# Optimization experiments

Measured on AMD Instinct MI355X. Metric: run time of the kernel, lower is better.

## Reference

```python
import jax, jax.numpy as jnp
import numpy as np

BS, NQ, D = 4, 12500, 256
HEADS, LEVELS, POINTS = 8, 2, 4
HD = D // HEADS
D_FF = 2048
SHAPES = ((100, 100), (50, 50))   # (H, W) per level; sum(H*W) == NQ
STARTS = (0, 10000)


def layer_norm(x, g, b, eps=1e-5):
    m = x.mean(-1, keepdims=True)
    v = ((x - m) ** 2).mean(-1, keepdims=True)
    return (x - m) * jax.lax.rsqrt(v + eps) * g + b


def bilinear_sample(value_l, loc, H, W):
    # value_l: (bs, heads, H*W, hd); loc: (bs, heads, nq, P, 2) normalized [0,1]
    # matches F.grid_sample(align_corners=False, padding_mode='zeros')
    x = loc[..., 0] * W - 0.5
    y = loc[..., 1] * H - 0.5
    x0 = jnp.floor(x)
    y0 = jnp.floor(y)
    wx1 = x - x0
    wy1 = y - y0
    wx0 = 1.0 - wx1
    wy0 = 1.0 - wy1
    x0i = x0.astype(jnp.int32)
    y0i = y0.astype(jnp.int32)

    def gather(xi, yi):
        valid = (xi >= 0) & (xi < W) & (yi >= 0) & (yi < H)
        idx = jnp.clip(yi, 0, H - 1) * W + jnp.clip(xi, 0, W - 1)  # (bs,heads,nq,P)
        b, h, nq, P = idx.shape
        g = jnp.take_along_axis(value_l, idx.reshape(b, h, nq * P, 1), axis=2)
        g = g.reshape(b, h, nq, P, -1)
        return g * valid[..., None].astype(g.dtype)

    g00 = gather(x0i, y0i)
    g10 = gather(x0i + 1, y0i)
    g01 = gather(x0i, y0i + 1)
    g11 = gather(x0i + 1, y0i + 1)
    return (g00 * (wx0 * wy0)[..., None] + g10 * (wx1 * wy0)[..., None]
            + g01 * (wx0 * wy1)[..., None] + g11 * (wx1 * wy1)[..., None])


def setup_inputs() -> dict:
    key = jax.random.key(0)
    ks = jax.random.split(key, 20)
    s = 0.02
    inp = {
        'query': jax.random.normal(ks[0], (BS, NQ, D), jnp.float32),
        'reference_points': jax.random.uniform(ks[1], (BS, NQ, LEVELS, 2), jnp.float32),
        'w_off': s * jax.random.normal(ks[2], (D, HEADS * LEVELS * POINTS * 2), jnp.float32),
        'b_off': s * jax.random.normal(ks[3], (HEADS * LEVELS * POINTS * 2,), jnp.float32),
        'w_attn': s * jax.random.normal(ks[4], (D, HEADS * LEVELS * POINTS), jnp.float32),
        'b_attn': s * jax.random.normal(ks[5], (HEADS * LEVELS * POINTS,), jnp.float32),
        'w_val': s * jax.random.normal(ks[6], (D, D), jnp.float32),
        'b_val': jnp.zeros((D,), jnp.float32),
        'w_out': s * jax.random.normal(ks[7], (D, D), jnp.float32),
        'b_out': jnp.zeros((D,), jnp.float32),
        'w1': s * jax.random.normal(ks[8], (D, D_FF), jnp.float32),
        'b1': jnp.zeros((D_FF,), jnp.float32),
        'w2': s * jax.random.normal(ks[9], (D_FF, D), jnp.float32),
        'b2': jnp.zeros((D,), jnp.float32),
        'ln0_g': jnp.ones((D,), jnp.float32),
        'ln0_b': jnp.zeros((D,), jnp.float32),
        'ln1_g': jnp.ones((D,), jnp.float32),
        'ln1_b': jnp.zeros((D,), jnp.float32),
    }
    return inp


def reference(query, reference_points, w_off, b_off, w_attn, b_attn, w_val, b_val,
              w_out, b_out, w1, b1, w2, b2, ln0_g, ln0_b, ln1_g, ln1_b):
    bs, nq, _ = query.shape
    # value projection; encoder self-attention: value == query tokens
    value = (query @ w_val + b_val).reshape(bs, nq, HEADS, HD).transpose(0, 2, 1, 3)  # (bs,heads,nv,hd)
    off = (query @ w_off + b_off).reshape(bs, nq, HEADS, LEVELS, POINTS, 2)
    aw = (query @ w_attn + b_attn).reshape(bs, nq, HEADS, LEVELS * POINTS)
    aw = jax.nn.softmax(aw, axis=-1).reshape(bs, nq, HEADS, LEVELS, POINTS)

    out = jnp.zeros((bs, HEADS, nq, HD), query.dtype)
    for l, (H, W) in enumerate(SHAPES):
        normalizer = jnp.array([W, H], query.dtype)
        # (bs,nq,heads,P,2)
        loc = reference_points[:, :, None, l, None, :] + off[:, :, :, l] / normalizer
        loc = loc.transpose(0, 2, 1, 3, 4)  # (bs,heads,nq,P,2)
        v_l = value[:, :, STARTS[l]:STARTS[l] + H * W]  # (bs,heads,H*W,hd)
        sampled = bilinear_sample(v_l, loc, H, W)       # (bs,heads,nq,P,hd)
        w_l = aw[:, :, :, l].transpose(0, 2, 1, 3)      # (bs,heads,nq,P)
        out = out + (sampled * w_l[..., None]).sum(axis=3)

    attn_out = out.transpose(0, 2, 1, 3).reshape(bs, nq, D) @ w_out + b_out
    x = layer_norm(query + attn_out, ln0_g, ln0_b)
    h = jax.nn.relu(x @ w1 + b1)
    x = layer_norm(x + (h @ w2 + b2), ln1_g, ln1_b)
    return x
```

## Files before the change

kernel.cpp:

```cpp
#include <hip/hip_runtime.h>


#define NQv 12500
#define BSv 4
#define Dv  256
#define DFF 2048

typedef __attribute__((ext_vector_type(8))) __bf16 bf16x8;
typedef __attribute__((ext_vector_type(4))) float f32x4;

__device__ __forceinline__ ushort f32_to_bf16(float f) {
  unsigned u = __float_as_uint(f);
  u += 0x7FFFu + ((u >> 16) & 1u);
  return (ushort)(u >> 16);
}
__device__ __forceinline__ float bf16_to_f32(ushort u) {
  return __uint_as_float(((unsigned)u) << 16);
}

__global__ __launch_bounds__(256) void conv_bf16_kernel(
    const float* __restrict__ in, ushort* __restrict__ out, int n4) {
  int i = blockIdx.x * 256 + threadIdx.x;
  if (i >= n4) return;
  float4 v = reinterpret_cast<const float4*>(in)[i];
  uint2 st;
  st.x = (unsigned)f32_to_bf16(v.x) | ((unsigned)f32_to_bf16(v.y) << 16);
  st.y = (unsigned)f32_to_bf16(v.z) | ((unsigned)f32_to_bf16(v.w) << 16);
  reinterpret_cast<uint2*>(out)[i] = st;
}

__global__ __launch_bounds__(256) void ttrans_kernel(
    const float* __restrict__ in, ushort* __restrict__ out, int K, int N) {
  __shared__ ushort tl[64][65];
  const int n0 = blockIdx.x * 64, k0 = blockIdx.y * 64;
  const int t = threadIdx.x;
#pragma unroll
  for (int i = 0; i < 16; ++i) {
    int idx = t + 256 * i;
    int r = idx >> 6, c = idx & 63;
    tl[r][c] = f32_to_bf16(in[(size_t)(k0 + r) * N + n0 + c]);
  }
  __syncthreads();
#pragma unroll
  for (int i = 0; i < 16; ++i) {
    int idx = t + 256 * i;
    int r = idx >> 6, c = idx & 63;
    out[(size_t)(n0 + r) * K + k0 + c] = tl[c][r];
  }
}

__global__ __launch_bounds__(256) void build_wcat_kernel(
    const float* __restrict__ w_val, const float* __restrict__ w_off,
    const float* __restrict__ w_attn, const float* __restrict__ b_val,
    const float* __restrict__ b_off, const float* __restrict__ b_attn,
    ushort* __restrict__ wcat, float* __restrict__ bcat) {
  int i = blockIdx.x * 256 + threadIdx.x;
  if (i < 448 * 256) {
    int n = i >> 8, k = i & 255;
    float v = (n < 256) ? w_val[(size_t)k * 256 + n]
              : (n < 384) ? w_off[(size_t)k * 128 + (n - 256)]
                          : w_attn[(size_t)k * 64 + (n - 384)];
    wcat[i] = f32_to_bf16(v);
  }
  if (i < 512)
    bcat[i] = (i < 256) ? b_val[i] : (i < 384) ? b_off[i - 256]
              : (i < 448) ? b_attn[i - 384] : 0.f;
}

template <int MODE>
__global__ __launch_bounds__(256) void stagefmt_kernel(
    const ushort* __restrict__ src, ushort* __restrict__ dst) {
  int i = blockIdx.x * 256 + threadIdx.x;
  int g = i >> 10, c = i & 1023;
  int srcrow, srck;
  if (MODE == 0) { srcrow = (g >> 2) * 128 + (c & 127); srck = (g & 3) * 64 + ((c >> 7) & 7) * 8; }
  if (MODE == 1) { srcrow = c & 255; srck = (g >> 2) * 128 + (g & 3) * 32 + ((c >> 8) & 3) * 8; }
  if (MODE == 2) { srcrow = c & 255; srck = g * 32 + ((c >> 8) & 3) * 8; }
  const int LD = (MODE == 1) ? 2048 : 256;
  *reinterpret_cast<uint4*>(dst + (size_t)i * 8) =
      *reinterpret_cast<const uint4*>(src + (size_t)srcrow * LD + srck);
}

#define TBM 128
#define TBN 128
#define TBK 32

template <int RELU, int NMASK, int SPLIT>
__global__ __launch_bounds__(256) void gemm128_kernel(
    const ushort* __restrict__ A, const ushort* __restrict__ Bt,
    const float* __restrict__ bias, ushort* __restrict__ C,
    ushort* __restrict__ C2,
    int M, int K, int ldc, int Nreal) {
  __shared__ ushort lds[4][TBM * TBK];

  const int t = threadIdx.x;
  const int wid = t >> 6, lane = t & 63;
  const int wr = wid >> 1, wc = wid & 1;
  const int m0 = blockIdx.y * TBM;
  const int n0 = blockIdx.x * TBN;

  int srowA[2], srowB[2], gsl[2];
#pragma unroll
  for (int i = 0; i < 2; i++) {
    int row = i * 64 + (t >> 2);
    int ar = m0 + row;
    srowA[i] = (ar < M) ? ar : (M - 1);
    srowB[i] = n0 + row;
    gsl[i] = ((t & 3) ^ ((row >> 1) & 3)) * 8;
  }

  f32x4 acc[4][4] = {};
  const int nt = K / TBK;
  int cur = 0;

#pragma unroll
  for (int i = 0; i < 2; i++) {
    const int ldsoff = (i * 256 + wid * 64) * 8;
    __builtin_amdgcn_global_load_lds(
        (const __attribute__((address_space(1))) void*)(A + (size_t)srowA[i] * K + gsl[i]),
        (__attribute__((address_space(3))) void*)(lds[0] + ldsoff), 16, 0, 0);
    __builtin_amdgcn_global_load_lds(
        (const __attribute__((address_space(1))) void*)(Bt + (size_t)srowB[i] * K + gsl[i]),
        (__attribute__((address_space(3))) void*)(lds[1] + ldsoff), 16, 0, 0);
  }
  __syncthreads();

  const int rl = lane & 15, kh = lane >> 4;
  for (int tk = 0; tk < nt; ++tk) {
    if (tk + 1 < nt) {
      const int k0 = (tk + 1) * TBK;
      const int nb = (cur ^ 1) * 2;
#pragma unroll
      for (int i = 0; i < 2; i++) {
        const int ldsoff = (i * 256 + wid * 64) * 8;
        __builtin_amdgcn_global_load_lds(
            (const __attribute__((address_space(1))) void*)(A + (size_t)srowA[i] * K + k0 + gsl[i]),
            (__attribute__((address_space(3))) void*)(lds[nb] + ldsoff), 16, 0, 0);
        __builtin_amdgcn_global_load_lds(
            (const __attribute__((address_space(1))) void*)(Bt + (size_t)srowB[i] * K + k0 + gsl[i]),
            (__attribute__((address_space(3))) void*)(lds[nb + 1] + ldsoff), 16, 0, 0);
      }
    }
    {
      const ushort* As = lds[cur * 2];
      const ushort* Bs = lds[cur * 2 + 1];
      bf16x8 afr[4], bfr[4];
#pragma unroll
      for (int ni = 0; ni < 4; ni++) {
        int rowb = wc * 64 + ni * 16 + rl;
        int p = kh ^ ((rowb >> 1) & 3);
        bfr[ni] = *reinterpret_cast<const bf16x8*>(Bs + rowb * 32 + p * 8);
      }
#pragma unroll
      for (int mi = 0; mi < 4; mi++) {
        int rowa = wr * 64 + mi * 16 + rl;
        int p = kh ^ ((rowa >> 1) & 3);
        afr[mi] = *reinterpret_cast<const bf16x8*>(As + rowa * 32 + p * 8);
      }
#pragma unroll
      for (int mi = 0; mi < 4; mi++)
#pragma unroll
        for (int ni = 0; ni < 4; ni++)
          acc[mi][ni] = __builtin_amdgcn_mfma_f32_16x16x32_bf16(afr[mi], bfr[ni], acc[mi][ni], 0, 0, 0);
    }
    __syncthreads();
    cur ^= 1;
  }

  ushort* ldsC = lds[0];
  const int rgrp = lane >> 4, cl = lane & 15;
#pragma unroll
  for (int pass = 0; pass < 2; ++pass) {
    if (wr == pass) {
#pragma unroll
      for (int mi = 0; mi < 4; mi++) {
#pragma unroll
        for (int ni = 0; ni < 4; ni++) {
          int col = wc * 64 + ni * 16 + cl;
          float bv = bias[n0 + col];
#pragma unroll
          for (int r = 0; r < 4; r++) {
            int rloc = mi * 16 + rgrp * 4 + r;
            float v = acc[mi][ni][r] + bv;
            if (RELU) v = fmaxf(v, 0.f);
            ldsC[rloc * 132 + col] = f32_to_bf16(v);
          }
        }
      }
    }
    __syncthreads();
    {
      int rloc = t >> 2;
      int row = m0 + pass * 64 + rloc;
      if (row < M) {
#pragma unroll
        for (int j = 0; j < 4; j++) {
          int col = (t & 3) * 32 + j * 8;
          uint4 v = *reinterpret_cast<const uint4*>(ldsC + rloc * 132 + col);
          if (SPLIT) {
            int gcol = n0 + col;
            if (gcol < 256)
              *reinterpret_cast<uint4*>(C + (size_t)row * 256 + gcol) = v;
            else if (gcol < 448)
              *reinterpret_cast<uint4*>(C2 + (size_t)row * 192 + (gcol - 256)) = v;
          } else if (!NMASK || n0 + col < Nreal) {
            *reinterpret_cast<uint4*>(C + (size_t)row * ldc + n0 + col) = v;
          }
        }
      }
    }
    __syncthreads();
  }
}

__global__ __launch_bounds__(256, 2) void outproj_ln0_kernel(
    const ushort* __restrict__ samp,
    const ushort* __restrict__ wqf,
    const float* __restrict__ bias,
    const float* __restrict__ query,
    const float* __restrict__ g0, const float* __restrict__ be0,
    ushort* __restrict__ xb,
    int M) {
  __shared__ ushort lds_all[32768];
  ushort* As = lds_all;
  ushort* ring0 = lds_all + 16384;

  const int t = threadIdx.x;
  const int wv = t >> 6;
  const int lane = t & 63;
  const int rl = lane & 15, kq = lane >> 4;
  const int cl = lane & 15, g4 = lane >> 4;
  const int m0 = blockIdx.x * 64;

  ushort* ring[2] = {ring0, ring0 + 8192};

  auto issueB = [&](int j, ushort* dst) {
#pragma unroll
    for (int ii = 0; ii < 4; ++ii) {
      int c = t + 256 * ii;
      __builtin_amdgcn_global_load_lds(
          (const __attribute__((address_space(1))) void*)(wqf + (size_t)j * 8192 + (size_t)c * 8),
          (__attribute__((address_space(3))) void*)(dst + (size_t)c * 8), 16, 0, 0);
    }
  };

#pragma unroll
  for (int ii = 0; ii < 8; ++ii) {
    int c = t + 256 * ii;
    __builtin_amdgcn_global_load_lds(
        (const __attribute__((address_space(1))) void*)(
            samp + (size_t)blockIdx.x * 16384 + (size_t)c * 8),
        (__attribute__((address_space(3))) void*)(As + (size_t)c * 8), 16, 0, 0);
  }
  issueB(0, ring[0]);
  __syncthreads();

  f32x4 accF[4][4] = {};
  int cur = 0;

#pragma unroll
  for (int j = 0; j < 8; ++j) {
    if (j + 1 < 8) issueB(j + 1, ring[cur ^ 1]);
    const ushort* Bs = ring[cur];
    bf16x8 afr[4], bfr[4];
#pragma unroll
    for (int mi = 0; mi < 4; mi++)
      afr[mi] = *reinterpret_cast<const bf16x8*>(As + (j * 4 + kq) * 512 + (mi * 16 + rl) * 8);
#pragma unroll
    for (int ni = 0; ni < 4; ni++)
      bfr[ni] = *reinterpret_cast<const bf16x8*>(Bs + kq * 2048 + (wv * 64 + ni * 16 + rl) * 8);
    __builtin_amdgcn_s_setprio(1);
#pragma unroll
    for (int mi = 0; mi < 4; mi++)
#pragma unroll
      for (int ni = 0; ni < 4; ni++)
        accF[mi][ni] = __builtin_amdgcn_mfma_f32_16x16x32_bf16(afr[mi], bfr[ni], accF[mi][ni], 0, 0, 0);
    __builtin_amdgcn_s_setprio(0);
    __syncthreads();
    cur ^= 1;
  }

  float* ptab = (float*)ring0;
  float* mtab = (float*)(ring0 + 2048);

  float bc[4], gc[4], bec[4];
#pragma unroll
  for (int ni = 0; ni < 4; ni++) {
    int col = wv * 64 + ni * 16 + cl;
    bc[ni] = bias[col]; gc[ni] = g0[col]; bec[ni] = be0[col];
  }
#pragma unroll
  for (int mi = 0; mi < 4; mi++) {
#pragma unroll
    for (int ni = 0; ni < 4; ni++) {
      int col = wv * 64 + ni * 16 + cl;
#pragma unroll
      for (int r = 0; r < 4; r++) {
        int row = mi * 16 + g4 * 4 + r;
        int qrow = m0 + row; qrow = (qrow < M) ? qrow : (M - 1);
        accF[mi][ni][r] += bc[ni] + query[(size_t)qrow * 256 + col];
      }
    }
  }
#pragma unroll
  for (int mi = 0; mi < 4; mi++) {
#pragma unroll
    for (int r = 0; r < 4; r++) {
      float s = accF[mi][0][r] + accF[mi][1][r] + accF[mi][2][r] + accF[mi][3][r];
      float sq = accF[mi][0][r] * accF[mi][0][r] + accF[mi][1][r] * accF[mi][1][r] +
                 accF[mi][2][r] * accF[mi][2][r] + accF[mi][3][r] * accF[mi][3][r];
#pragma unroll
      for (int o = 1; o < 16; o <<= 1) {
        s += __shfl_xor(s, o, 64);
        sq += __shfl_xor(sq, o, 64);
      }
      if (cl == 0) {
        int row = mi * 16 + g4 * 4 + r;
        ptab[(row * 4 + wv) * 2 + 0] = s;
        ptab[(row * 4 + wv) * 2 + 1] = sq;
      }
    }
  }
  __syncthreads();
  {
    int row = t >> 2, part = t & 3;
    float s = ptab[(row * 4 + part) * 2 + 0];
    float sq = ptab[(row * 4 + part) * 2 + 1];
    s += __shfl_xor(s, 1, 64);  sq += __shfl_xor(sq, 1, 64);
    s += __shfl_xor(s, 2, 64);  sq += __shfl_xor(sq, 2, 64);
    if (part == 0) {
      float mean = s * (1.f / 256.f);
      float var = sq * (1.f / 256.f) - mean * mean;
      mtab[row * 2 + 0] = mean;
      mtab[row * 2 + 1] = rsqrtf(var + 1e-5f);
    }
  }
  __syncthreads();
#pragma unroll
  for (int mi = 0; mi < 4; mi++) {
#pragma unroll
    for (int r = 0; r < 4; r++) {
      int row = mi * 16 + g4 * 4 + r;
      float2 ms = *reinterpret_cast<const float2*>(mtab + row * 2);
      int grow = m0 + row;
      if (grow < M) {
        size_t base = (size_t)(grow >> 7) * 32768 + (size_t)(grow & 127) * 8;
#pragma unroll
        for (int ni = 0; ni < 4; ni++) {
          int col = wv * 64 + ni * 16 + cl;
          xb[base + (size_t)(col >> 3) * 1024 + (col & 7)] =
              f32_to_bf16((accF[mi][ni][r] - ms.x) * ms.y * gc[ni] + bec[ni]);
        }
      }
    }
  }
}

__global__ __launch_bounds__(512, 1) void ffn_ln_fused_kernel(
    const ushort* __restrict__ xb,
    const ushort* __restrict__ w1f,
    const float* __restrict__ b1,
    const ushort* __restrict__ w2f,
    const float* __restrict__ b2,
    const float* __restrict__ g1, const float* __restrict__ be1,
    float* __restrict__ out, int M) {
  __shared__ ushort lds_all[73856];
  ushort* As = lds_all;
  ushort* Hs = lds_all + 32768;
  ushort* stg0 = lds_all + 49280;

  const int t = threadIdx.x;
  const int wv = t >> 6;
  const int wm = wv >> 2;
  const int wn = wv & 3;
  const int lane = t & 63;
  const int rl = lane & 15, kq = lane >> 4;
  const int cl = lane & 15, g4 = lane >> 4;
  const int m0 = blockIdx.x * 128;

  auto stg = [&](int i) { return stg0 + i * 8192; };

  auto issueB1 = [&](int p, int j, ushort* dst) {
    const ushort* src = w1f + (size_t)(p * 4 + j) * 8192;
#pragma unroll
    for (int ii = 0; ii < 2; ++ii) {
      int c = t + 512 * ii;
      __builtin_amdgcn_global_load_lds(
          (const __attribute__((address_space(1))) void*)(src + (size_t)c * 8),
          (__attribute__((address_space(3))) void*)(dst + (size_t)c * 8), 16, 0, 0);
    }
  };
  auto issueB2 = [&](int p, int tt, ushort* dst) {
    const ushort* src = w2f + (size_t)(p * 4 + tt) * 8192;
#pragma unroll
    for (int ii = 0; ii < 2; ++ii) {
      int c = t + 512 * ii;
      __builtin_amdgcn_global_load_lds(
          (const __attribute__((address_space(1))) void*)(src + (size_t)c * 8),
          (__attribute__((address_space(3))) void*)(dst + (size_t)c * 8), 16, 0, 0);
    }
  };

#pragma unroll
  for (int ii = 0; ii < 8; ++ii) {
    int c = t + 512 * ii;
    __builtin_amdgcn_global_load_lds(
        (const __attribute__((address_space(1))) void*)(
            xb + (size_t)blockIdx.x * 32768 + (size_t)c * 8),
        (__attribute__((address_space(3))) void*)(As + (size_t)c * 8), 16, 0, 0);
  }
  issueB1(0, 0, stg(0));
  issueB1(0, 1, stg(1));
  asm volatile("s_waitcnt vmcnt(2)" ::: "memory");
  __builtin_amdgcn_s_barrier();

  f32x4 acc1[4][2] = {};
  f32x4 accF[4][4] = {};
  int cur = 0;

  for (int p = 0; p < 16; ++p) {
#pragma unroll
    for (int j = 0; j < 8; ++j) {
      int tgt = cur + 2; if (tgt >= 3) tgt -= 3;
      if (j <= 5) {
        const int j2 = j + 2;
        const int p2 = p + (j2 >> 3);
        if ((j2 & 7) < 4) issueB1(p2, j2 & 3, stg(tgt));
        else issueB2(p2, (j2 & 7) - 4, stg(tgt));
        asm volatile("s_waitcnt vmcnt(4) lgkmcnt(0)" ::: "memory");
      } else if (p < 15) {
        const int j2m = (j + 2) & 7;
        issueB1(p + 1, j2m, stg(tgt));
        asm volatile("s_waitcnt vmcnt(4) lgkmcnt(0)" ::: "memory");
      } else if (j == 6) {
        asm volatile("s_waitcnt vmcnt(2) lgkmcnt(0)" ::: "memory");
      } else {
        asm volatile("s_waitcnt vmcnt(0) lgkmcnt(0)" ::: "memory");
      }
      __builtin_amdgcn_s_barrier();
      __builtin_amdgcn_sched_barrier(0);

      const ushort* Bs = stg(cur);
      if (j < 4) {
        __builtin_amdgcn_s_setprio(1);
#pragma unroll
        for (int kk = 0; kk < 2; ++kk) {
          bf16x8 afr[4], bfr[2];
          const int slotA = j * 8 + kk * 4 + kq;
#pragma unroll
          for (int mi = 0; mi < 4; mi++)
            afr[mi] = *reinterpret_cast<const bf16x8*>(
                As + slotA * 1024 + (wm * 64 + mi * 16 + rl) * 8);
          const int slotB = kk * 4 + kq;
#pragma unroll
          for (int ni = 0; ni < 2; ni++)
            bfr[ni] = *reinterpret_cast<const bf16x8*>(
                Bs + slotB * 1024 + (wn * 32 + ni * 16 + rl) * 8);
#pragma unroll
          for (int mi = 0; mi < 4; mi++)
#pragma unroll
            for (int ni = 0; ni < 2; ni++)
              acc1[mi][ni] = __builtin_amdgcn_mfma_f32_16x16x32_bf16(afr[mi], bfr[ni], acc1[mi][ni], 0, 0, 0);
        }
        __builtin_amdgcn_s_setprio(0);
        if (j == 3) {
#pragma unroll
          for (int ni = 0; ni < 2; ni++) {
            int col = wn * 32 + ni * 16 + cl;
            float b1v = b1[p * 128 + col];
            const int s = col >> 3, w8 = col & 7;
#pragma unroll
            for (int mi = 0; mi < 4; mi++) {
#pragma unroll
              for (int r = 0; r < 4; r++) {
                int row = wm * 64 + mi * 16 + g4 * 4 + r;
                Hs[s * 1032 + row * 8 + w8] = f32_to_bf16(fmaxf(acc1[mi][ni][r] + b1v, 0.f));
              }
            }
          }
#pragma unroll
          for (int mi = 0; mi < 4; mi++)
#pragma unroll
            for (int ni = 0; ni < 2; ni++)
              acc1[mi][ni] = (f32x4){0.f, 0.f, 0.f, 0.f};
        }
      } else {
        const int tt = j - 4;
        bf16x8 a2f[4], b2f[4];
#pragma unroll
        for (int mi = 0; mi < 4; mi++)
          a2f[mi] = *reinterpret_cast<const bf16x8*>(
              Hs + (tt * 4 + kq) * 1032 + (wm * 64 + mi * 16 + rl) * 8);
#pragma unroll
        for (int ni = 0; ni < 4; ni++)
          b2f[ni] = *reinterpret_cast<const bf16x8*>(
              Bs + kq * 2048 + (wn * 64 + ni * 16 + rl) * 8);
        __builtin_amdgcn_s_setprio(1);
#pragma unroll
        for (int mi = 0; mi < 4; mi++)
#pragma unroll
          for (int ni = 0; ni < 4; ni++)
            accF[mi][ni] = __builtin_amdgcn_mfma_f32_16x16x32_bf16(a2f[mi], b2f[ni], accF[mi][ni], 0, 0, 0);
        __builtin_amdgcn_s_setprio(0);
      }
      cur = cur + 1; if (cur >= 3) cur -= 3;
    }
  }

  float* ptab = (float*)stg0;
  float* mtab = (float*)(stg0 + 2048);

  float b2c[4], g1c[4], bec[4];
#pragma unroll
  for (int ni = 0; ni < 4; ni++) {
    int col = wn * 64 + ni * 16 + cl;
    b2c[ni] = b2[col]; g1c[ni] = g1[col]; bec[ni] = be1[col];
  }
#pragma unroll
  for (int mi = 0; mi < 4; mi++) {
#pragma unroll
    for (int ni = 0; ni < 4; ni++) {
      int col = wn * 64 + ni * 16 + cl;
#pragma unroll
      for (int r = 0; r < 4; r++) {
        int row = wm * 64 + mi * 16 + g4 * 4 + r;
        ushort xv = As[(col >> 3) * 1024 + row * 8 + (col & 7)];
        accF[mi][ni][r] += b2c[ni] + bf16_to_f32(xv);
      }
    }
  }
#pragma unroll
  for (int mi = 0; mi < 4; mi++) {
#pragma unroll
    for (int r = 0; r < 4; r++) {
      float s = accF[mi][0][r] + accF[mi][1][r] + accF[mi][2][r] + accF[mi][3][r];
      float sq = accF[mi][0][r] * accF[mi][0][r] + accF[mi][1][r] * accF[mi][1][r] +
                 accF[mi][2][r] * accF[mi][2][r] + accF[mi][3][r] * accF[mi][3][r];
#pragma unroll
      for (int o = 1; o < 16; o <<= 1) {
        s += __shfl_xor(s, o, 64);
        sq += __shfl_xor(sq, o, 64);
      }
      if (cl == 0) {
        int row = wm * 64 + mi * 16 + g4 * 4 + r;
        ptab[(row * 4 + wn) * 2 + 0] = s;
        ptab[(row * 4 + wn) * 2 + 1] = sq;
      }
    }
  }
  __syncthreads();
  {
    int row = t >> 2, part = t & 3;
    float s = ptab[(row * 4 + part) * 2 + 0];
    float sq = ptab[(row * 4 + part) * 2 + 1];
    s += __shfl_xor(s, 1, 64);  sq += __shfl_xor(sq, 1, 64);
    s += __shfl_xor(s, 2, 64);  sq += __shfl_xor(sq, 2, 64);
    if (part == 0) {
      float mean = s * (1.f / 256.f);
      float var = sq * (1.f / 256.f) - mean * mean;
      mtab[row * 2 + 0] = mean;
      mtab[row * 2 + 1] = rsqrtf(var + 1e-5f);
    }
  }
  __syncthreads();
#pragma unroll
  for (int mi = 0; mi < 4; mi++) {
#pragma unroll
    for (int r = 0; r < 4; r++) {
      int row = wm * 64 + mi * 16 + g4 * 4 + r;
      float2 ms = *reinterpret_cast<const float2*>(mtab + row * 2);
      int grow = m0 + row;
      if (grow < M) {
#pragma unroll
        for (int ni = 0; ni < 4; ni++) {
          int col = wn * 64 + ni * 16 + cl;
          out[(size_t)grow * 256 + col] = (accF[mi][ni][r] - ms.x) * ms.y * g1c[ni] + bec[ni];
        }
      }
    }
  }
}

__global__ __launch_bounds__(256) void deform_attn_kernel(
    const ushort* __restrict__ val,
    const ushort* __restrict__ oa,
    const float* __restrict__ refp,
    ushort* __restrict__ out,
    int total)
{
  int tid = blockIdx.x * 256 + threadIdx.x;
  if (tid >= total) return;
  int c = tid & 3;
  int idx = tid >> 2;
  int h = idx & 7;
  int row = idx >> 3;
  int bl = row / NQv;

  const ushort* orow = oa + (size_t)row * 192;

  uint lraw = *reinterpret_cast<const uint*>(orow + 128 + h * 8 + c * 2);
  float l0 = bf16_to_f32((ushort)(lraw & 0xffffu));
  float l1 = bf16_to_f32((ushort)(lraw >> 16));
  float mx = fmaxf(l0, l1);
  mx = fmaxf(mx, __shfl_xor(mx, 1, 64));
  mx = fmaxf(mx, __shfl_xor(mx, 2, 64));
  float e0 = __expf(l0 - mx), e1 = __expf(l1 - mx);
  float sm = e0 + e1;
  sm += __shfl_xor(sm, 1, 64);
  sm += __shfl_xor(sm, 2, 64);
  float inv = 1.f / sm;

  ushort o4[4];
  *reinterpret_cast<uint2*>(o4) = *reinterpret_cast<const uint2*>(orow + h * 16 + c * 4);
  float4 rp = *reinterpret_cast<const float4*>(refp + (size_t)row * 4);
  float Wl = (c & 2) ? 50.f : 100.f;
  float fx = ((c & 2) ? rp.z : rp.x) * Wl - 0.5f;
  float fy = ((c & 2) ? rp.w : rp.y) * Wl - 0.5f;
  float myx0 = fx + bf16_to_f32(o4[0]);
  float myy0 = fy + bf16_to_f32(o4[1]);
  float myx1 = fx + bf16_to_f32(o4[2]);
  float myy1 = fy + bf16_to_f32(o4[3]);
  float myw0 = e0 * inv, myw1 = e1 * inv;

  const int lanebase = (threadIdx.x & 63) & ~3;
  float acc8[8] = {};
#pragma unroll
  for (int p = 0; p < 8; ++p) {
    const int src = lanebase | (p >> 1);
    float x = __shfl((p & 1) ? myx1 : myx0, src, 64);
    float y = __shfl((p & 1) ? myy1 : myy0, src, 64);
    float w = __shfl((p & 1) ? myw1 : myw0, src, 64);
    const int W = (p < 4) ? 100 : 50, H = W;
    const ushort* vbase = val + ((size_t)bl * NQv + ((p < 4) ? 0 : 10000)) * 256 + h * 32 + c * 8;
    float x0f = floorf(x), y0f = floorf(y);
    float wx1 = x - x0f, wy1 = y - y0f;
    float wx0 = 1.f - wx1, wy0 = 1.f - wy1;
    int x0 = (int)x0f, y0 = (int)y0f;
    float cw[4] = {w * wx0 * wy0, w * wx1 * wy0, w * wx0 * wy1, w * wx1 * wy1};
    int cx[4] = {x0, x0 + 1, x0, x0 + 1};
    int cy[4] = {y0, y0, y0 + 1, y0 + 1};
#pragma unroll
    for (int cc = 0; cc < 4; cc++) {
      int xi = cx[cc], yi = cy[cc];
      if (xi >= 0 && xi < W && yi >= 0 && yi < H) {
        ushort vr[8];
        *reinterpret_cast<uint4*>(vr) =
            *reinterpret_cast<const uint4*>(vbase + (size_t)(yi * W + xi) * 256);
        float ww = cw[cc];
#pragma unroll
        for (int j = 0; j < 8; j++) acc8[j] += ww * bf16_to_f32(vr[j]);
      }
    }
  }

  ushort st[8];
#pragma unroll
  for (int j = 0; j < 8; j++) st[j] = f32_to_bf16(acc8[j]);
  *reinterpret_cast<uint4*>(out + (size_t)(row >> 6) * 16384 +
                            (size_t)(h * 4 + c) * 512 + (size_t)(row & 63) * 8) =
      *reinterpret_cast<uint4*>(st);
}

extern "C" void kernel_launch(void* const* d_in, const int* in_sizes, int n_in,
                              void* d_out, int out_size, void* d_ws, size_t ws_size,
                              hipStream_t stream) {
  const float* query  = (const float*)d_in[0];
  const float* refp   = (const float*)d_in[1];
  const float* w_off  = (const float*)d_in[2];
  const float* b_off  = (const float*)d_in[3];
  const float* w_attn = (const float*)d_in[4];
  const float* b_attn = (const float*)d_in[5];
  const float* w_val  = (const float*)d_in[6];
  const float* b_val  = (const float*)d_in[7];
  const float* w_out  = (const float*)d_in[8];
  const float* b_out  = (const float*)d_in[9];
  const float* w1     = (const float*)d_in[10];
  const float* b1     = (const float*)d_in[11];
  const float* w2     = (const float*)d_in[12];
  const float* b2     = (const float*)d_in[13];
  const float* ln0g   = (const float*)d_in[14];
  const float* ln0b   = (const float*)d_in[15];
  const float* ln1g   = (const float*)d_in[16];
  const float* ln1b   = (const float*)d_in[17];
  float* outp = (float*)d_out;

  char* ws = (char*)d_ws;
  size_t woff = 0;
  auto walloc = [&](size_t bytes) { size_t r = woff; woff += (bytes + 255) & ~(size_t)255; return r; };
  ushort* wcat = (ushort*)(ws + walloc((size_t)512 * 256 * 2));
  float*  bcat = (float*)(ws + walloc(512 * 4));
  ushort* wqt  = (ushort*)(ws + walloc((size_t)256 * 256 * 2));
  ushort* w1t  = (ushort*)(ws + walloc((size_t)DFF * 256 * 2));
  ushort* w2t  = (ushort*)(ws + walloc((size_t)256 * DFF * 2));
  ushort* wqf  = (ushort*)(ws + walloc((size_t)8 * 8192 * 2));
  ushort* w1f  = (ushort*)(ws + walloc((size_t)64 * 8192 * 2));
  ushort* w2f  = (ushort*)(ws + walloc((size_t)64 * 8192 * 2));
  char* arena = ws + woff;
  size_t arena_sz = (ws_size > woff) ? (ws_size - woff) : 0;

  int nb = ((size_t)BSv * NQv * 1920 + (4u << 20) <= arena_sz) ? BSv : 1;
  const int R = nb * NQv;
  const size_t xbsz = (size_t)((R + 127) / 128) * 65536;
  const size_t smsz = (size_t)((R + 63) / 64) * 32768;
  ushort* qb   = (ushort*)arena;
  ushort* valb = (ushort*)(arena + xbsz);
  ushort* oab  = (ushort*)(arena + xbsz + (size_t)R * 512);
  ushort* samp = (ushort*)(arena + xbsz + (size_t)R * 512 + (size_t)R * 384);
  ushort* xb   = qb;

  build_wcat_kernel<<<dim3(448), dim3(256), 0, stream>>>(
      w_val, w_off, w_attn, b_val, b_off, b_attn, wcat, bcat);
  ttrans_kernel<<<dim3(4, 4), dim3(256), 0, stream>>>(w_out, wqt, Dv, Dv);
  ttrans_kernel<<<dim3(DFF / 64, 4), dim3(256), 0, stream>>>(w1, w1t, Dv, DFF);
  ttrans_kernel<<<dim3(4, DFF / 64), dim3(256), 0, stream>>>(w2, w2t, DFF, Dv);
  stagefmt_kernel<2><<<dim3(32), dim3(256), 0, stream>>>(wqt, wqf);
  stagefmt_kernel<0><<<dim3(256), dim3(256), 0, stream>>>(w1t, w1f);
  stagefmt_kernel<1><<<dim3(256), dim3(256), 0, stream>>>(w2t, w2f);

  const int MT = (R + TBM - 1) / TBM;

  for (int c = 0; c < BSv / nb; c++) {
    const int row0 = c * R;
    const float* qrow = query + (size_t)row0 * Dv;

    conv_bf16_kernel<<<dim3((R * 64 + 255) / 256), dim3(256), 0, stream>>>(qrow, qb, R * 64);

    gemm128_kernel<0, 1, 1><<<dim3(4, MT), dim3(256), 0, stream>>>(
        qb, wcat, bcat, valb, oab, R, Dv, 448, 448);

    deform_attn_kernel<<<dim3((R * 32 + 255) / 256), dim3(256), 0, stream>>>(
        valb, oab, refp + (size_t)row0 * 4, samp, R * 32);

    outproj_ln0_kernel<<<dim3((R + 63) / 64), dim3(256), 0, stream>>>(
        samp, wqf, b_out, qrow, ln0g, ln0b, xb, R);

    ffn_ln_fused_kernel<<<dim3((R + 127) / 128), dim3(512), 0, stream>>>(
        xb, w1f, b1, w2f, b2, ln1g, ln1b, outp + (size_t)row0 * 256, R);
  }
}
```

Before: 332.0 us.

## Stage output stores through LDS and remap GEMM workgroups across XCDs

Three changes target memory traffic. The QKV/offset GEMM remaps its workgroup IDs so that consecutive tiles land on the same XCD, improving L2 locality. The out-projection+LN0 epilogue and the deformable-attention kernel now write results into LDS and then emit coalesced 16-byte stores into the tiled layout, replacing scattered stores. This costs an extra barrier and LDS round trip in each kernel, and the xb store in outproj uses a blockIdx-derived base that assumes 64-row blocks.

```diff
diff --git a/kernel.cpp b/kernel.cpp
--- a/kernel.cpp
+++ b/kernel.cpp
@@ -96,8 +96,14 @@
   const int t = threadIdx.x;
   const int wid = t >> 6, lane = t & 63;
   const int wr = wid >> 1, wc = wid & 1;
-  const int m0 = blockIdx.y * TBM;
-  const int n0 = blockIdx.x * TBN;
+
+  const int nwg = gridDim.x * gridDim.y;
+  const int lbid = blockIdx.y * gridDim.x + blockIdx.x;
+  const int q = nwg >> 3, r = nwg & 7;
+  const int xcd = lbid & 7, li = lbid >> 3;
+  const int wgid = (xcd < r ? xcd * (q + 1) : r * (q + 1) + (xcd - r) * q) + li;
+  const int m0 = (wgid / gridDim.x) * TBM;
+  const int n0 = (wgid % gridDim.x) * TBN;
 
   int srowA[2], srowB[2], gsl[2];
 #pragma unroll
@@ -342,28 +348,33 @@
     for (int r = 0; r < 4; r++) {
       int row = mi * 16 + g4 * 4 + r;
       float2 ms = *reinterpret_cast<const float2*>(mtab + row * 2);
-      int grow = m0 + row;
-      if (grow < M) {
-        size_t base = (size_t)(grow >> 7) * 32768 + (size_t)(grow & 127) * 8;
-#pragma unroll
-        for (int ni = 0; ni < 4; ni++) {
-          int col = wv * 64 + ni * 16 + cl;
-          xb[base + (size_t)(col >> 3) * 1024 + (col & 7)] =
-              f32_to_bf16((accF[mi][ni][r] - ms.x) * ms.y * gc[ni] + bec[ni]);
-        }
-      }
+#pragma unroll
+      for (int ni = 0; ni < 4; ni++) {
+        int col = wv * 64 + ni * 16 + cl;
+        As[(col >> 3) * 512 + row * 8 + (col & 7)] =
+            f32_to_bf16((accF[mi][ni][r] - ms.x) * ms.y * gc[ni] + bec[ni]);
+      }
+    }
+  }
+  __syncthreads();
+  {
+    const size_t base128 = (size_t)(blockIdx.x >> 1) * 32768 + (size_t)(blockIdx.x & 1) * 512;
+#pragma unroll
+    for (int ii = 0; ii < 8; ++ii) {
+      int c = t + 256 * ii;
+      int s = c >> 6, rl2 = c & 63;
+      if (m0 + rl2 < M)
+        *reinterpret_cast<uint4*>(xb + base128 + (size_t)s * 1024 + (size_t)rl2 * 8) =
+            *reinterpret_cast<const uint4*>(As + (size_t)c * 8);
     }
   }
 }
 
 __global__ __launch_bounds__(512, 1) void ffn_ln_fused_kernel(
-    const ushort* __restrict__ xb,
-    const ushort* __restrict__ w1f,
-    const float* __restrict__ b1,
-    const ushort* __restrict__ w2f,
-    const float* __restrict__ b2,
-    const float* __restrict__ g1, const float* __restrict__ be1,
-    float* __restrict__ out, int M) {
+    const ushort* __restrict__ xb, const ushort* __restrict__ w1f,
+    const float* __restrict__ b1, const ushort* __restrict__ w2f,
+    const float* __restrict__ b2, const float* __restrict__ g1,
+    const float* __restrict__ be1, float* __restrict__ out, int M) {
   __shared__ ushort lds_all[73856];
   ushort* As = lds_all;
   ushort* Hs = lds_all + 32768;
@@ -586,79 +597,92 @@
     const ushort* __restrict__ oa,
     const float* __restrict__ refp,
     ushort* __restrict__ out,
-    int total)
-{
-  int tid = blockIdx.x * 256 + threadIdx.x;
-  if (tid >= total) return;
-  int c = tid & 3;
-  int idx = tid >> 2;
-  int h = idx & 7;
-  int row = idx >> 3;
-  int bl = row / NQv;
-
-  const ushort* orow = oa + (size_t)row * 192;
-
-  uint lraw = *reinterpret_cast<const uint*>(orow + 128 + h * 8 + c * 2);
-  float l0 = bf16_to_f32((ushort)(lraw & 0xffffu));
-  float l1 = bf16_to_f32((ushort)(lraw >> 16));
-  float mx = fmaxf(l0, l1);
-  mx = fmaxf(mx, __shfl_xor(mx, 1, 64));
-  mx = fmaxf(mx, __shfl_xor(mx, 2, 64));
-  float e0 = __expf(l0 - mx), e1 = __expf(l1 - mx);
-  float sm = e0 + e1;
-  sm += __shfl_xor(sm, 1, 64);
-  sm += __shfl_xor(sm, 2, 64);
-  float inv = 1.f / sm;
-
-  ushort o4[4];
-  *reinterpret_cast<uint2*>(o4) = *reinterpret_cast<const uint2*>(orow + h * 16 + c * 4);
-  float4 rp = *reinterpret_cast<const float4*>(refp + (size_t)row * 4);
-  float Wl = (c & 2) ? 50.f : 100.f;
-  float fx = ((c & 2) ? rp.z : rp.x) * Wl - 0.5f;
-  float fy = ((c & 2) ? rp.w : rp.y) * Wl - 0.5f;
-  float myx0 = fx + bf16_to_f32(o4[0]);
-  float myy0 = fy + bf16_to_f32(o4[1]);
-  float myx1 = fx + bf16_to_f32(o4[2]);
-  float myy1 = fy + bf16_to_f32(o4[3]);
-  float myw0 = e0 * inv, myw1 = e1 * inv;
-
-  const int lanebase = (threadIdx.x & 63) & ~3;
-  float acc8[8] = {};
-#pragma unroll
-  for (int p = 0; p < 8; ++p) {
-    const int src = lanebase | (p >> 1);
-    float x = __shfl((p & 1) ? myx1 : myx0, src, 64);
-    float y = __shfl((p & 1) ? myy1 : myy0, src, 64);
-    float w = __shfl((p & 1) ? myw1 : myw0, src, 64);
-    const int W = (p < 4) ? 100 : 50, H = W;
-    const ushort* vbase = val + ((size_t)bl * NQv + ((p < 4) ? 0 : 10000)) * 256 + h * 32 + c * 8;
-    float x0f = floorf(x), y0f = floorf(y);
-    float wx1 = x - x0f, wy1 = y - y0f;
-    float wx0 = 1.f - wx1, wy0 = 1.f - wy1;
-    int x0 = (int)x0f, y0 = (int)y0f;
-    float cw[4] = {w * wx0 * wy0, w * wx1 * wy0, w * wx0 * wy1, w * wx1 * wy1};
-    int cx[4] = {x0, x0 + 1, x0, x0 + 1};
-    int cy[4] = {y0, y0, y0 + 1, y0 + 1};
-#pragma unroll
-    for (int cc = 0; cc < 4; cc++) {
-      int xi = cx[cc], yi = cy[cc];
-      if (xi >= 0 && xi < W && yi >= 0 && yi < H) {
-        ushort vr[8];
-        *reinterpret_cast<uint4*>(vr) =
-            *reinterpret_cast<const uint4*>(vbase + (size_t)(yi * W + xi) * 256);
-        float ww = cw[cc];
-#pragma unroll
-        for (int j = 0; j < 8; j++) acc8[j] += ww * bf16_to_f32(vr[j]);
-      }
-    }
-  }
-
-  ushort st[8];
-#pragma unroll
-  for (int j = 0; j < 8; j++) st[j] = f32_to_bf16(acc8[j]);
-  *reinterpret_cast<uint4*>(out + (size_t)(row >> 6) * 16384 +
-                            (size_t)(h * 4 + c) * 512 + (size_t)(row & 63) * 8) =
-      *reinterpret_cast<uint4*>(st);
+    int R) {
+  __shared__ ushort repack[2048];
+
+  const int t = threadIdx.x;
+  const int c = t & 3;
+  const int h = (t >> 2) & 7;
+  const int rloc = t >> 5;
+  const int row0 = blockIdx.x * 8;
+  const int row = row0 + rloc;
+
+  if (row < R) {
+    const int bl = row / NQv;
+    const ushort* orow = oa + (size_t)row * 192;
+
+    uint lraw = *reinterpret_cast<const uint*>(orow + 128 + h * 8 + c * 2);
+    float l0 = bf16_to_f32((ushort)(lraw & 0xffffu));
+    float l1 = bf16_to_f32((ushort)(lraw >> 16));
+    float mx = fmaxf(l0, l1);
+    mx = fmaxf(mx, __shfl_xor(mx, 1, 64));
+    mx = fmaxf(mx, __shfl_xor(mx, 2, 64));
+    float e0 = __expf(l0 - mx), e1 = __expf(l1 - mx);
+    float sm = e0 + e1;
+    sm += __shfl_xor(sm, 1, 64);
+    sm += __shfl_xor(sm, 2, 64);
+    float inv = 1.f / sm;
+
+    ushort o4[4];
+    *reinterpret_cast<uint2*>(o4) = *reinterpret_cast<const uint2*>(orow + h * 16 + c * 4);
+    float4 rp = *reinterpret_cast<const float4*>(refp + (size_t)row * 4);
+    float Wl = (c & 2) ? 50.f : 100.f;
+    float fx = ((c & 2) ? rp.z : rp.x) * Wl - 0.5f;
+    float fy = ((c & 2) ? rp.w : rp.y) * Wl - 0.5f;
+    float myx0 = fx + bf16_to_f32(o4[0]);
+    float myy0 = fy + bf16_to_f32(o4[1]);
+    float myx1 = fx + bf16_to_f32(o4[2]);
+    float myy1 = fy + bf16_to_f32(o4[3]);
+    float myw0 = e0 * inv, myw1 = e1 * inv;
+
+    const int lanebase = (t & 63) & ~3;
+    float acc8[8] = {};
+#pragma unroll
+    for (int p = 0; p < 8; ++p) {
+      const int src = lanebase | (p >> 1);
+      float x = __shfl((p & 1) ? myx1 : myx0, src, 64);
+      float y = __shfl((p & 1) ? myy1 : myy0, src, 64);
+      float w = __shfl((p & 1) ? myw1 : myw0, src, 64);
+      const int W = (p < 4) ? 100 : 50, H = W;
+      const ushort* vbase = val + ((size_t)bl * NQv + ((p < 4) ? 0 : 10000)) * 256 + h * 32 + c * 8;
+      float x0f = floorf(x), y0f = floorf(y);
+      float wx1 = x - x0f, wy1 = y - y0f;
+      float wx0 = 1.f - wx1, wy0 = 1.f - wy1;
+      int x0 = (int)x0f, y0 = (int)y0f;
+      float cw[4] = {w * wx0 * wy0, w * wx1 * wy0, w * wx0 * wy1, w * wx1 * wy1};
+      int cx[4] = {x0, x0 + 1, x0, x0 + 1};
+      int cy[4] = {y0, y0, y0 + 1, y0 + 1};
+#pragma unroll
+      for (int cc = 0; cc < 4; cc++) {
+        int xi = cx[cc], yi = cy[cc];
+        if (xi >= 0 && xi < W && yi >= 0 && yi < H) {
+          ushort vr[8];
+          *reinterpret_cast<uint4*>(vr) =
+              *reinterpret_cast<const uint4*>(vbase + (size_t)(yi * W + xi) * 256);
+          float ww = cw[cc];
+#pragma unroll
+          for (int j = 0; j < 8; j++) acc8[j] += ww * bf16_to_f32(vr[j]);
+        }
+      }
+    }
+
+    ushort st[8];
+#pragma unroll
+    for (int j = 0; j < 8; j++) st[j] = f32_to_bf16(acc8[j]);
+    *reinterpret_cast<uint4*>(repack + (size_t)(h * 4 + c) * 64 + (size_t)rloc * 8) =
+        *reinterpret_cast<uint4*>(st);
+  }
+  __syncthreads();
+
+  {
+    int s2 = t >> 3, r2 = t & 7;
+    int grow = row0 + r2;
+    if (grow < R) {
+      int b64 = row0 >> 6, inner = (row0 & 63) + r2;
+      *reinterpret_cast<uint4*>(out + (size_t)b64 * 16384 + (size_t)s2 * 512 + (size_t)inner * 8) =
+          *reinterpret_cast<const uint4*>(repack + (size_t)s2 * 64 + (size_t)r2 * 8);
+    }
+  }
 }
 
 extern "C" void kernel_launch(void* const* d_in, const int* in_sizes, int n_in,
@@ -701,7 +725,6 @@
   int nb = ((size_t)BSv * NQv * 1920 + (4u << 20) <= arena_sz) ? BSv : 1;
   const int R = nb * NQv;
   const size_t xbsz = (size_t)((R + 127) / 128) * 65536;
-  const size_t smsz = (size_t)((R + 63) / 64) * 32768;
   ushort* qb   = (ushort*)arena;
   ushort* valb = (ushort*)(arena + xbsz);
   ushort* oab  = (ushort*)(arena + xbsz + (size_t)R * 512);
@@ -728,8 +751,8 @@
     gemm128_kernel<0, 1, 1><<<dim3(4, MT), dim3(256), 0, stream>>>(
         qb, wcat, bcat, valb, oab, R, Dv, 448, 448);
 
-    deform_attn_kernel<<<dim3((R * 32 + 255) / 256), dim3(256), 0, stream>>>(
-        valb, oab, refp + (size_t)row0 * 4, samp, R * 32);
+    deform_attn_kernel<<<dim3((R + 7) / 8), dim3(256), 0, stream>>>(
+        valb, oab, refp + (size_t)row0 * 4, samp, R);
 
     outproj_ln0_kernel<<<dim3((R + 63) / 64), dim3(256), 0, stream>>>(
         samp, wqf, b_out, qrow, ln0g, ln0b, xb, R);
```

New measurement: 323.5 us. 2.6% less time.
